# Kernel tuning notes

Measured on AMD Instinct MI355X. Metric: run time of the kernel, lower is better.

## Reference

```python
import jax, jax.numpy as jnp
import numpy as np

NUM_HEADS = 16
HEAD_DIM = 128  # hidden_size=2048 // num_heads=16


def setup_inputs() -> dict:
    key = jax.random.key(0)
    k1, k2, k3, k4, k5 = jax.random.split(key, 5)
    B, S, H = 4, 4096, 2048
    scale_in = 1.0 / np.sqrt(H)
    return {
        "x": jax.random.normal(k1, (B, S, H), dtype=jnp.float32),
        "Wqkv": jax.random.normal(k2, (H, 3 * H), dtype=jnp.float32) * scale_in,
        "bqkv": jax.random.normal(k3, (3 * H,), dtype=jnp.float32) * 0.01,
        "Wproj": jax.random.normal(k4, (H, H), dtype=jnp.float32) * scale_in,
        "bproj": jax.random.normal(k5, (H,), dtype=jnp.float32) * 0.01,
    }


def reference(x, Wqkv, bqkv, Wproj, bproj):
    B, S, hidden = x.shape
    H, D = NUM_HEADS, HEAD_DIM
    qkv = x @ Wqkv + bqkv                       # (B, S, 3*hidden)
    qkv = qkv.reshape(B, S, 3, H, D)
    q, k, v = qkv[:, :, 0], qkv[:, :, 1], qkv[:, :, 2]  # each (B, S, H, D)
    # Faithful to source: matmul over last two dims -> scores are (B, S, H, H)
    # (head-to-head attention per position; the repo never moved heads to dim 1).
    scores = jnp.einsum("bshd,bstd->bsht", q, k) / jnp.sqrt(jnp.asarray(D, x.dtype))
    weights = jax.nn.softmax(scores, axis=-1)    # (B, S, H, H)
    context = jnp.einsum("bsht,bstd->bshd", weights, v)  # (B, S, H, D)
    # Faithful reproduction of context.transpose(1, 2).contiguous().view(B, S, hidden)
    context = context.transpose(0, 2, 1, 3).reshape(B, S, hidden)
    return context @ Wproj + bproj
```

## Files before the change

### kernel.cpp

```cpp
#include <hip/hip_runtime.h>

typedef unsigned short u16;
typedef __attribute__((ext_vector_type(8))) short short8;
typedef __attribute__((ext_vector_type(4))) short short4v;
typedef __attribute__((ext_vector_type(4))) float float4v;

__device__ __forceinline__ u16 f2b(float f) {
  union { float f; unsigned u; } v; v.f = f;
  unsigned r = v.u + 0x7fffu + ((v.u >> 16) & 1u);
  return (u16)(r >> 16);
}

#define AS1(p) ((const __attribute__((address_space(1))) void*)(p))
#define AS3(p) ((__attribute__((address_space(3))) void*)(p))

__global__ __launch_bounds__(256) void cvt_bf16_kernel(const float* __restrict__ in,
                                                       u16* __restrict__ out, long n) {
  long i = ((long)blockIdx.x * 256 + threadIdx.x) * 8;
  if (i + 8 > n) return;
  float4v a = *(const float4v*)(in + i);
  float4v b = *(const float4v*)(in + i + 4);
  short8 o;
  o[0] = (short)f2b(a[0]); o[1] = (short)f2b(a[1]);
  o[2] = (short)f2b(a[2]); o[3] = (short)f2b(a[3]);
  o[4] = (short)f2b(b[0]); o[5] = (short)f2b(b[1]);
  o[6] = (short)f2b(b[2]); o[7] = (short)f2b(b[3]);
  *(short8*)(out + i) = o;
}

__global__ __launch_bounds__(256) void transpose_cvt_kernel(const float* __restrict__ in,
                                                            u16* __restrict__ out,
                                                            int rows, int cols) {
  __shared__ float tile[32][33];
  int bx = blockIdx.x * 32;
  int by = blockIdx.y * 32;
  int tx = threadIdx.x & 31, ty = threadIdx.x >> 5;
  for (int r = ty; r < 32; r += 8)
    tile[r][tx] = in[(long)(by + r) * cols + bx + tx];
  __syncthreads();
  for (int r = ty; r < 32; r += 8)
    out[(long)(bx + r) * rows + by + tx] = f2b(tile[tx][r]);
}

__global__ __launch_bounds__(256, 2) void gemm_bt_bias(const u16* __restrict__ A,
                                                       const u16* __restrict__ B,
                                                       const float* __restrict__ bias,
                                                       void* __restrict__ Cout,
                                                       int M, int N, int K, int out_bf16) {
  __shared__ __align__(16) u16 As[128 * 32];
  __shared__ __align__(16) u16 Bs[128 * 32];
  const int t = threadIdx.x;
  const int lane = t & 63;
  const int w = t >> 6;
  const int wm = w >> 1, wn = w & 1;
  const int lm = lane & 15, lq = lane >> 4;
  const long row0 = (long)blockIdx.y * 128;
  const long col0 = (long)blockIdx.x * 128;
  float4v acc[4][4] = {};

  const int u0 = t, u1 = t + 256;
  const u16* Ag0 = A + (row0 + (u0 >> 2)) * K + (u0 & 3) * 8;
  const u16* Ag1 = A + (row0 + (u1 >> 2)) * K + (u1 & 3) * 8;
  const u16* Bg0 = B + (col0 + (u0 >> 2)) * K + (u0 & 3) * 8;
  const u16* Bg1 = B + (col0 + (u1 >> 2)) * K + (u1 & 3) * 8;
  u16* lA0 = As + u0 * 8;  u16* lA1 = As + u1 * 8;
  u16* lB0 = Bs + u0 * 8;  u16* lB1 = Bs + u1 * 8;

  for (int kb = 0; kb < K; kb += 32) {
    __builtin_amdgcn_global_load_lds(AS1(Ag0 + kb), AS3(lA0), 16, 0, 0);
    __builtin_amdgcn_global_load_lds(AS1(Ag1 + kb), AS3(lA1), 16, 0, 0);
    __builtin_amdgcn_global_load_lds(AS1(Bg0 + kb), AS3(lB0), 16, 0, 0);
    __builtin_amdgcn_global_load_lds(AS1(Bg1 + kb), AS3(lB1), 16, 0, 0);
    __syncthreads();
    short8 af[4], bf[4];
#pragma unroll
    for (int i = 0; i < 4; i++)
      af[i] = *(const short8*)(As + (wm * 64 + i * 16 + lm) * 32 + lq * 8);
#pragma unroll
    for (int i = 0; i < 4; i++)
      bf[i] = *(const short8*)(Bs + (wn * 64 + i * 16 + lm) * 32 + lq * 8);
#pragma unroll
    for (int mt = 0; mt < 4; mt++)
#pragma unroll
      for (int nt = 0; nt < 4; nt++)
        acc[mt][nt] = __builtin_amdgcn_mfma_f32_16x16x32_bf16(af[mt], bf[nt], acc[mt][nt], 0, 0, 0);
    __syncthreads();
  }

#pragma unroll
  for (int nt = 0; nt < 4; nt++) {
    long cg = col0 + wn * 64 + nt * 16 + lm;
    float bv = bias[cg];
#pragma unroll
    for (int mt = 0; mt < 4; mt++) {
      long rbase = row0 + wm * 64 + mt * 16 + lq * 4;
#pragma unroll
      for (int r = 0; r < 4; r++) {
        float v = acc[mt][nt][r] + bv;
        long idx = (rbase + r) * N + cg;
        if (out_bf16) ((u16*)Cout)[idx] = f2b(v);
        else          ((float*)Cout)[idx] = v;
      }
    }
  }
}

__global__ __launch_bounds__(256) void head_attn_kernel(const u16* __restrict__ qkv,
                                                        u16* __restrict__ ctx) {
  __shared__ __align__(16) u16 vt_s[4][128 * 16];
  __shared__ __align__(16) u16 ws_s[4][16 * 32];
  const int tid = threadIdx.x;
  const int lane = tid & 63;
  const int w = tid >> 6;
  const int lm = lane & 15, lq = lane >> 4;
  const int pos = blockIdx.x * 4 + w;
  const int b = pos >> 12, s = pos & 4095;
  const long rowb = (long)pos * 6144;

  u16* vt = vt_s[w];
  u16* wsp = ws_s[w];

  for (int i = lane; i < 16 * 32; i += 64) wsp[i] = 0;

  {
    int tt = lane >> 2, db = (lane & 3) * 32;
#pragma unroll
    for (int c = 0; c < 4; c++) {
      short8 vv = *(const short8*)(qkv + rowb + 4096 + tt * 128 + db + c * 8);
#pragma unroll
      for (int j = 0; j < 8; j++)
        vt[(db + c * 8 + j) * 16 + tt] = (u16)vv[j];
    }
  }
  __syncthreads();

  float4v st = {0.f, 0.f, 0.f, 0.f};
#pragma unroll
  for (int ks = 0; ks < 4; ks++) {
    short8 qa = *(const short8*)(qkv + rowb + lm * 128 + ks * 32 + lq * 8);
    short8 kb = *(const short8*)(qkv + rowb + 2048 + lm * 128 + ks * 32 + lq * 8);
    st = __builtin_amdgcn_mfma_f32_16x16x32_bf16(qa, kb, st, 0, 0, 0);
  }

  const float sc = 0.08838834764831845f * 1.4426950408889634f;
#pragma unroll
  for (int r = 0; r < 4; r++) {
    float z = st[r] * sc;
    float m = z;
    m = fmaxf(m, __shfl_xor(m, 1));
    m = fmaxf(m, __shfl_xor(m, 2));
    m = fmaxf(m, __shfl_xor(m, 4));
    m = fmaxf(m, __shfl_xor(m, 8));
    float p = exp2f(z - m);
    float ss = p;
    ss += __shfl_xor(ss, 1);
    ss += __shfl_xor(ss, 2);
    ss += __shfl_xor(ss, 4);
    ss += __shfl_xor(ss, 8);
    wsp[(lq * 4 + r) * 32 + lm] = f2b(p / ss);
  }
  __syncthreads();

  short8 wa = *(const short8*)(wsp + lm * 32 + lq * 8);
#pragma unroll
  for (int dt = 0; dt < 8; dt++) {
    short8 vb = *(const short8*)(vt + (dt * 16 + lm) * 16 + (lq & 1) * 8);
    float4v o = {0.f, 0.f, 0.f, 0.f};
    o = __builtin_amdgcn_mfma_f32_16x16x32_bf16(wa, vb, o, 0, 0, 0);
#pragma unroll
    for (int r = 0; r < 4; r++) {
      int h = lq * 4 + r;
      ctx[(((long)(b * 16 + h) * 4096 + s) * 128) + dt * 16 + lm] = f2b(o[r]);
    }
  }
}

extern "C" void kernel_launch(void* const* d_in, const int* in_sizes, int n_in,
                              void* d_out, int out_size, void* d_ws, size_t ws_size,
                              hipStream_t stream) {
  const float* x     = (const float*)d_in[0];
  const float* Wqkv  = (const float*)d_in[1];
  const float* bqkv  = (const float*)d_in[2];
  const float* Wproj = (const float*)d_in[3];
  const float* bproj = (const float*)d_in[4];
  float* out = (float*)d_out;

  u16* xb     = (u16*)d_ws;
  u16* WqkvT  = xb + 33554432L;
  u16* WprojT = WqkvT + 12582912L;
  u16* qkvb   = WprojT + 4194304L;
  u16* ctxb   = qkvb + 100663296L;

  cvt_bf16_kernel<<<33554432L / 2048, 256, 0, stream>>>(x, xb, 33554432L);
  transpose_cvt_kernel<<<dim3(6144 / 32, 2048 / 32), 256, 0, stream>>>(Wqkv, WqkvT, 2048, 6144);
  transpose_cvt_kernel<<<dim3(2048 / 32, 2048 / 32), 256, 0, stream>>>(Wproj, WprojT, 2048, 2048);

  gemm_bt_bias<<<dim3(6144 / 128, 16384 / 128), 256, 0, stream>>>(
      xb, WqkvT, bqkv, qkvb, 16384, 6144, 2048, 1);

  head_attn_kernel<<<4096, 256, 0, stream>>>(qkvb, ctxb);

  gemm_bt_bias<<<dim3(2048 / 128, 16384 / 128), 256, 0, stream>>>(
      ctxb, WprojT, bproj, out, 16384, 2048, 2048, 0);
}
```

Before: 983.5 us.

## Replace GEMM with 256x256 double-buffered, swizzled, XCD-remapped 8-wave kernel

```diff
diff --git a/kernel.cpp b/kernel.cpp
--- a/kernel.cpp
+++ b/kernel.cpp
@@ -2,7 +2,6 @@
 
 typedef unsigned short u16;
 typedef __attribute__((ext_vector_type(8))) short short8;
-typedef __attribute__((ext_vector_type(4))) short short4v;
 typedef __attribute__((ext_vector_type(4))) float float4v;
 
 __device__ __forceinline__ u16 f2b(float f) {
@@ -13,6 +12,7 @@
 
 #define AS1(p) ((const __attribute__((address_space(1))) void*)(p))
 #define AS3(p) ((__attribute__((address_space(3))) void*)(p))
+#define MFMA16(a, b, c) __builtin_amdgcn_mfma_f32_16x16x32_bf16(a, b, c, 0, 0, 0)
 
 __global__ __launch_bounds__(256) void cvt_bf16_kernel(const float* __restrict__ in,
                                                        u16* __restrict__ out, long n) {
@@ -42,62 +42,144 @@
     out[(long)(bx + r) * rows + by + tx] = f2b(tile[tx][r]);
 }
 
-__global__ __launch_bounds__(256, 2) void gemm_bt_bias(const u16* __restrict__ A,
-                                                       const u16* __restrict__ B,
-                                                       const float* __restrict__ bias,
-                                                       void* __restrict__ Cout,
-                                                       int M, int N, int K, int out_bf16) {
-  __shared__ __align__(16) u16 As[128 * 32];
-  __shared__ __align__(16) u16 Bs[128 * 32];
+__global__ __launch_bounds__(512, 2) void gemm256_bt_bias(const u16* __restrict__ A,
+                                                          const u16* __restrict__ B,
+                                                          const float* __restrict__ bias,
+                                                          void* __restrict__ Cout,
+                                                          int M, int N, int K, int out_bf16) {
+  __shared__ __align__(16) u16 As[2][2][8192];
+  __shared__ __align__(16) u16 Bs[2][2][8192];
+
   const int t = threadIdx.x;
   const int lane = t & 63;
   const int w = t >> 6;
-  const int wm = w >> 1, wn = w & 1;
-  const int lm = lane & 15, lq = lane >> 4;
-  const long row0 = (long)blockIdx.y * 128;
-  const long col0 = (long)blockIdx.x * 128;
-  float4v acc[4][4] = {};
-
-  const int u0 = t, u1 = t + 256;
-  const u16* Ag0 = A + (row0 + (u0 >> 2)) * K + (u0 & 3) * 8;
-  const u16* Ag1 = A + (row0 + (u1 >> 2)) * K + (u1 & 3) * 8;
-  const u16* Bg0 = B + (col0 + (u0 >> 2)) * K + (u0 & 3) * 8;
-  const u16* Bg1 = B + (col0 + (u1 >> 2)) * K + (u1 & 3) * 8;
-  u16* lA0 = As + u0 * 8;  u16* lA1 = As + u1 * 8;
-  u16* lB0 = Bs + u0 * 8;  u16* lB1 = Bs + u1 * 8;
-
-  for (int kb = 0; kb < K; kb += 32) {
-    __builtin_amdgcn_global_load_lds(AS1(Ag0 + kb), AS3(lA0), 16, 0, 0);
-    __builtin_amdgcn_global_load_lds(AS1(Ag1 + kb), AS3(lA1), 16, 0, 0);
-    __builtin_amdgcn_global_load_lds(AS1(Bg0 + kb), AS3(lB0), 16, 0, 0);
-    __builtin_amdgcn_global_load_lds(AS1(Bg1 + kb), AS3(lB1), 16, 0, 0);
-    __syncthreads();
-    short8 af[4], bf[4];
-#pragma unroll
-    for (int i = 0; i < 4; i++)
-      af[i] = *(const short8*)(As + (wm * 64 + i * 16 + lm) * 32 + lq * 8);
-#pragma unroll
-    for (int i = 0; i < 4; i++)
-      bf[i] = *(const short8*)(Bs + (wn * 64 + i * 16 + lm) * 32 + lq * 8);
-#pragma unroll
-    for (int mt = 0; mt < 4; mt++)
-#pragma unroll
-      for (int nt = 0; nt < 4; nt++)
-        acc[mt][nt] = __builtin_amdgcn_mfma_f32_16x16x32_bf16(af[mt], bf[nt], acc[mt][nt], 0, 0, 0);
-    __syncthreads();
-  }
-
-#pragma unroll
-  for (int nt = 0; nt < 4; nt++) {
-    long cg = col0 + wn * 64 + nt * 16 + lm;
-    float bv = bias[cg];
-#pragma unroll
-    for (int mt = 0; mt < 4; mt++) {
-      long rbase = row0 + wm * 64 + mt * 16 + lq * 4;
+  const int wm = w >> 2;
+  const int wn = w & 3;
+  const int lm = lane & 15;
+  const int lq = lane >> 4;
+
+  const int nwg = gridDim.x * gridDim.y;
+  const int orig = blockIdx.y * gridDim.x + blockIdx.x;
+  const int qq = nwg >> 3, rr = nwg & 7;
+  const int xcd = orig & 7, loc = orig >> 3;
+  const int wgid = (xcd < rr ? xcd * (qq + 1) : rr * (qq + 1) + (xcd - rr) * qq) + loc;
+  const int bx = wgid % gridDim.x;
+  const int by = wgid / gridDim.x;
+
+  const long row0 = (long)by * 256;
+  const long col0 = (long)bx * 256;
+
+  const int phys0 = t * 8;
+  const int phys1 = 4096 + t * 8;
+  const int log0 = phys0 ^ (((phys0 >> 8) & 1) << 4);
+  const int log1 = phys1 ^ (((phys1 >> 8) & 1) << 4);
+  const long r0s = log0 >> 6; const int c0s = log0 & 63;
+  const long r1s = log1 >> 6; const int c1s = log1 & 63;
+
+  const u16* Ag0 = A + (row0 + r0s) * K + c0s;
+  const u16* Ag1 = A + (row0 + r1s) * K + c1s;
+  const u16* Bg0 = B + (col0 + r0s) * K + c0s;
+  const u16* Bg1 = B + (col0 + r1s) * K + c1s;
+  const long hstride = 128L * (long)K;
+
+  const int sb = (lm * 64 + lq * 8) ^ (((lm >> 2) & 1) << 4);
+
+  float4v acc[8][4] = {};
+  const int NT = K >> 6;
+
+  auto stA = [&](int buf, int h, int kt) {
+    u16* d = &As[buf][h][0] + t * 8;
+    const long ko = (long)kt * 64 + (long)h * hstride;
+    __builtin_amdgcn_global_load_lds(AS1(Ag0 + ko), AS3(d), 16, 0, 0);
+    __builtin_amdgcn_global_load_lds(AS1(Ag1 + ko), AS3(d + 4096), 16, 0, 0);
+  };
+  auto stB = [&](int buf, int h, int kt) {
+    u16* d = &Bs[buf][h][0] + t * 8;
+    const long ko = (long)kt * 64 + (long)h * hstride;
+    __builtin_amdgcn_global_load_lds(AS1(Bg0 + ko), AS3(d), 16, 0, 0);
+    __builtin_amdgcn_global_load_lds(AS1(Bg1 + ko), AS3(d + 4096), 16, 0, 0);
+  };
+
+  auto ktile = [&](int buf, int u) {
+    asm volatile("" ::: "memory");
+    const u16* Ab = &As[buf][wm][0] + sb;
+    const u16* Bb = &Bs[buf][wn >> 1][0] + (wn & 1) * 4096 + sb;
+    const int kn  = (u + 1 < NT) ? u + 1 : NT - 1;
+    const int kb2 = (u + 2 < NT) ? u + 2 : NT - 1;
+
+    short8 bfr[4][2];
+#pragma unroll
+    for (int n = 0; n < 4; n++) {
+      bfr[n][0] = *(const short8*)(Bb + n * 1024);
+      bfr[n][1] = *(const short8*)(Bb + n * 1024 + 32);
+    }
+    {
+      short8 a00 = *(const short8*)(Ab + 0);
+      short8 a01 = *(const short8*)(Ab + 32);
+      short8 a10 = *(const short8*)(Ab + 1024);
+      short8 a11 = *(const short8*)(Ab + 1024 + 32);
+      stA(buf ^ 1, 0, kn);
+      asm volatile("s_waitcnt lgkmcnt(8)" ::: "memory");
+      __builtin_amdgcn_s_barrier();
+      asm volatile("s_waitcnt lgkmcnt(0)" ::: "memory");
+      __builtin_amdgcn_s_setprio(1);
+#pragma unroll
+      for (int n = 0; n < 4; n++) {
+        acc[0][n] = MFMA16(a00, bfr[n][0], acc[0][n]);
+        acc[0][n] = MFMA16(a01, bfr[n][1], acc[0][n]);
+        acc[1][n] = MFMA16(a10, bfr[n][0], acc[1][n]);
+        acc[1][n] = MFMA16(a11, bfr[n][1], acc[1][n]);
+      }
+      __builtin_amdgcn_s_setprio(0);
+      __builtin_amdgcn_s_barrier();
+    }
+#pragma unroll
+    for (int p = 1; p < 4; p++) {
+      short8 a00 = *(const short8*)(Ab + (2 * p) * 1024);
+      short8 a01 = *(const short8*)(Ab + (2 * p) * 1024 + 32);
+      short8 a10 = *(const short8*)(Ab + (2 * p + 1) * 1024);
+      short8 a11 = *(const short8*)(Ab + (2 * p + 1) * 1024 + 32);
+      if (p == 1)      stA(buf ^ 1, 1, kn);
+      else if (p == 2) stB(buf, 0, kb2);
+      else             stB(buf, 1, kb2);
+      __builtin_amdgcn_s_barrier();
+      asm volatile("s_waitcnt lgkmcnt(0)" ::: "memory");
+      __builtin_amdgcn_s_setprio(1);
+#pragma unroll
+      for (int n = 0; n < 4; n++) {
+        acc[2 * p][n]     = MFMA16(a00, bfr[n][0], acc[2 * p][n]);
+        acc[2 * p][n]     = MFMA16(a01, bfr[n][1], acc[2 * p][n]);
+        acc[2 * p + 1][n] = MFMA16(a10, bfr[n][0], acc[2 * p + 1][n]);
+        acc[2 * p + 1][n] = MFMA16(a11, bfr[n][1], acc[2 * p + 1][n]);
+      }
+      __builtin_amdgcn_s_setprio(0);
+      if (p == 3) asm volatile("s_waitcnt vmcnt(4)" ::: "memory");
+      __builtin_amdgcn_s_barrier();
+    }
+  };
+
+  stA(0, 0, 0); stA(0, 1, 0); stB(0, 0, 0); stB(0, 1, 0);
+  const int k1 = (NT > 1) ? 1 : 0;
+  stB(1, 0, k1); stB(1, 1, k1);
+  asm volatile("s_waitcnt vmcnt(4)" ::: "memory");
+  __builtin_amdgcn_s_barrier();
+
+  for (int u = 0; u < NT; u += 2) {
+    ktile(0, u);
+    ktile(1, u + 1);
+  }
+
+#pragma unroll
+  for (int n = 0; n < 4; n++) {
+    const long cg = col0 + wn * 64 + n * 16 + lm;
+    const float bv = bias[cg];
+#pragma unroll
+    for (int m = 0; m < 8; m++) {
+      const long rbase = row0 + wm * 128 + m * 16 + lq * 4;
 #pragma unroll
       for (int r = 0; r < 4; r++) {
-        float v = acc[mt][nt][r] + bv;
-        long idx = (rbase + r) * N + cg;
+        const float v = acc[m][n][r] + bv;
+        const long idx = (rbase + r) * N + cg;
         if (out_bf16) ((u16*)Cout)[idx] = f2b(v);
         else          ((float*)Cout)[idx] = v;
       }
@@ -195,11 +277,11 @@
   transpose_cvt_kernel<<<dim3(6144 / 32, 2048 / 32), 256, 0, stream>>>(Wqkv, WqkvT, 2048, 6144);
   transpose_cvt_kernel<<<dim3(2048 / 32, 2048 / 32), 256, 0, stream>>>(Wproj, WprojT, 2048, 2048);
 
-  gemm_bt_bias<<<dim3(6144 / 128, 16384 / 128), 256, 0, stream>>>(
+  gemm256_bt_bias<<<dim3(6144 / 256, 16384 / 256), 512, 0, stream>>>(
       xb, WqkvT, bqkv, qkvb, 16384, 6144, 2048, 1);
 
   head_attn_kernel<<<4096, 256, 0, stream>>>(qkvb, ctxb);
 
-  gemm_bt_bias<<<dim3(2048 / 128, 16384 / 128), 256, 0, stream>>>(
+  gemm256_bt_bias<<<dim3(2048 / 256, 16384 / 256), 512, 0, stream>>>(
       ctxb, WprojT, bproj, out, 16384, 2048, 2048, 0);
 }
```

Result: faster. 930.2 us (-5.4%).
